# Kernel tuning notes

Measured on AMD Instinct MI355X. Metric: run time of the kernel, lower is better.

Reference implementation:

```python
import jax, jax.numpy as jnp
import numpy as np
import math

B, D_MODEL, EMB, ORDER, SEQ = 4, 64, 33, 64, 256
TARGET, FAST_PCT, SLOW_PCT = 0.01, 0.3, 1.5


def _pos_emb(L, emb_dim):
    # PositionalEmbedding: t in [0,1], complex exponential bands
    t = jnp.linspace(0.0, 1.0, L)[None, :, None]                     # [1,L,1]
    bands = (emb_dim - 1) // 2
    t_r = jnp.linspace(0.0, L - 1.0, L)[None, :, None]
    w = 2.0 * math.pi * t_r / L
    f = jnp.linspace(1e-4, bands - 1.0, bands)[None, None]
    zc = jnp.exp(-1j * f * w)
    z = jnp.concatenate([t, zc.real, zc.imag], axis=-1)              # [1,L,emb_dim]
    return z.astype(jnp.float32), t.astype(jnp.float32)


def setup_inputs() -> dict:
    key = jax.random.key(0)
    ks = jax.random.split(key, 24)
    z, _ = _pos_emb(SEQ, EMB)

    def lin(k, fan_in, fan_out):
        return jax.random.normal(k, (fan_in, fan_out), jnp.float32) / np.sqrt(fan_in)

    inp = {
        'x': jax.random.normal(ks[0], (B, D_MODEL, SEQ, SEQ), jnp.float32),
        'z': z,
        'Xw1': lin(ks[1], EMB, ORDER), 'Xb1': jax.random.normal(ks[2], (ORDER,), jnp.float32) * 0.02,
        'Xw2': lin(ks[3], ORDER, ORDER), 'Xb2': jax.random.normal(ks[4], (ORDER,), jnp.float32) * 0.02,
        'Xw3': lin(ks[5], ORDER, ORDER), 'Xb3': jax.random.normal(ks[6], (ORDER,), jnp.float32) * 0.02,
        'Xwo': lin(ks[7], ORDER, D_MODEL),
        'Xfreq': jnp.ones((1, ORDER), jnp.float32),  # Sin freq, w=1, shared across layers
        'Yw1': lin(ks[8], EMB, ORDER), 'Yb1': jax.random.normal(ks[9], (ORDER,), jnp.float32) * 0.02,
        'Yw2': lin(ks[10], ORDER, ORDER), 'Yb2': jax.random.normal(ks[11], (ORDER,), jnp.float32) * 0.02,
        'Yw3': lin(ks[12], ORDER, ORDER), 'Yb3': jax.random.normal(ks[13], (ORDER,), jnp.float32) * 0.02,
        'Ywo': lin(ks[14], ORDER, D_MODEL),
        'Yfreq': jnp.ones((1, ORDER), jnp.float32),
        'bias': jax.random.normal(ks[15], (D_MODEL,), jnp.float32),
        'L': SEQ,
    }
    return inp


def _implicit_filter(z, w1, b1, w2, b2, w3, b3, wo, freq, t, deltas):
    # MLP with shared Sin activation, then exponential modulation (shift=0)
    h = jnp.sin(freq * (z @ w1 + b1))
    h = jnp.sin(freq * (h @ w2 + b2))
    h = jnp.sin(freq * (h @ w3 + b3))
    h = h @ wo                                   # [1,L,d_model]
    decay = jnp.exp(-t * jnp.abs(deltas))        # [1,L,d_model]
    return h * decay


def reference(x, z, Xw1, Xb1, Xw2, Xb2, Xw3, Xb3, Xwo, Xfreq,
              Yw1, Yb1, Yw2, Yb2, Yw3, Yb3, Ywo, Yfreq, bias, L):
    d_model = x.shape[1]
    t = jnp.linspace(0.0, 1.0, L)[None, :, None].astype(jnp.float32)
    max_dec = math.log(TARGET) / FAST_PCT
    min_dec = math.log(TARGET) / SLOW_PCT
    deltas = jnp.linspace(min_dec, max_dec, d_model)[None, None].astype(jnp.float32)

    hx = _implicit_filter(z, Xw1, Xb1, Xw2, Xb2, Xw3, Xb3, Xwo, Xfreq, t, deltas)
    hy = _implicit_filter(z, Yw1, Yb1, Yw2, Yb2, Yw3, Yb3, Ywo, Yfreq, t, deltas)
    # separable outer-product 2D kernel: [1,L,L,d_model] -> [d_model,L,L]
    k = jnp.einsum('ijk,imk->ijmk', hx, hy)[0]
    k = jnp.transpose(k, (2, 0, 1))

    fft_size = 2 * L
    k_f = jnp.fft.rfft2(k, s=(fft_size, fft_size)) / fft_size       # [D, 2L, L+1]
    u_f = jnp.fft.rfft2(x.astype(jnp.float32), s=(fft_size, fft_size))  # [B, D, 2L, L+1]
    y = jnp.fft.irfft2(u_f * k_f, s=(fft_size, fft_size))[..., :L, :L]
    out = y + x * bias[:, None, None]
    return out.astype(x.dtype)
```

## Files before the change

kernel.cpp:

```cpp
#include <hip/hip_runtime.h>

#define SL 256
#define RSTRIDE 312

typedef _Float16 f16;
typedef _Float16 f16x8 __attribute__((ext_vector_type(8)));
typedef _Float16 f16x4 __attribute__((ext_vector_type(4)));
typedef float f32x4 __attribute__((ext_vector_type(4)));

__global__ __launch_bounds__(64) void k_filters(
    const float* __restrict__ z,
    const float* __restrict__ Xw1, const float* __restrict__ Xb1,
    const float* __restrict__ Xw2, const float* __restrict__ Xb2,
    const float* __restrict__ Xw3, const float* __restrict__ Xb3,
    const float* __restrict__ Xwo, const float* __restrict__ Xfreq,
    const float* __restrict__ Yw1, const float* __restrict__ Yb1,
    const float* __restrict__ Yw2, const float* __restrict__ Yb2,
    const float* __restrict__ Yw3, const float* __restrict__ Yb3,
    const float* __restrict__ Ywo, const float* __restrict__ Yfreq,
    f16* __restrict__ hxT, f16* __restrict__ hyT)
{
    const int l = blockIdx.x;
    const int sel = blockIdx.y;
    const int t = threadIdx.x;
    const float* w1 = sel ? Yw1 : Xw1;  const float* b1 = sel ? Yb1 : Xb1;
    const float* w2 = sel ? Yw2 : Xw2;  const float* b2 = sel ? Yb2 : Xb2;
    const float* w3 = sel ? Yw3 : Xw3;  const float* b3 = sel ? Yb3 : Xb3;
    const float* wo = sel ? Ywo : Xwo;  const float* freq = sel ? Yfreq : Xfreq;
    f16* hT = sel ? hyT : hxT;

    __shared__ float zb[33];
    __shared__ float ha[64];
    __shared__ float hb[64];

    if (t < 33) zb[t] = z[l * 33 + t];
    __syncthreads();

    const float fr = freq[t];
    float s = b1[t];
    for (int k = 0; k < 33; ++k) s += zb[k] * w1[k * 64 + t];
    ha[t] = sinf(fr * s);
    __syncthreads();

    s = b2[t];
    for (int k = 0; k < 64; ++k) s += ha[k] * w2[k * 64 + t];
    hb[t] = sinf(fr * s);
    __syncthreads();

    s = b3[t];
    for (int k = 0; k < 64; ++k) s += hb[k] * w3[k * 64 + t];
    ha[t] = sinf(fr * s);
    __syncthreads();

    s = 0.f;
    for (int k = 0; k < 64; ++k) s += ha[k] * wo[k * 64 + t];

    const float MIN_DEC = -3.0701134573253937f;
    const float MAX_DEC = -15.350567286626968f;
    float ad = fabsf(MIN_DEC + (MAX_DEC - MIN_DEC) * ((float)t / 63.0f));
    float tl = (float)l / 255.0f;
    hT[t * 256 + l] = (f16)(s * expf(-tl * ad));
}

__device__ __forceinline__ f16x8 cvt8(float4 a, float4 b)
{
    f16x8 h;
    h[0] = (f16)a.x; h[1] = (f16)a.y; h[2] = (f16)a.z; h[3] = (f16)a.w;
    h[4] = (f16)b.x; h[5] = (f16)b.y; h[6] = (f16)b.z; h[7] = (f16)b.w;
    return h;
}

__device__ __forceinline__ void build_R(f16* R, const f16* __restrict__ hc,
                                        int tid)
{
    for (int idx = tid; idx < 8 * RSTRIDE; idx += 512) {
        int c = idx / RSTRIDE;
        int k = idx - c * RSTRIDE;
        int u = k + c;
        R[idx] = (u <= 255) ? hc[255 - u] : (f16)0.f;
    }
}

template<int J0>
__device__ __forceinline__ void phase1(
    const float* __restrict__ xr0, const float* __restrict__ xr1,
    const f16* __restrict__ R, f32x4 (&acc)[16], int ln, int quad)
{
    constexpr int QS = (J0 == 0) ? 4 : 8;
    float4 a0 = *(const float4*)xr0;
    float4 a1 = *(const float4*)(xr0 + 4);
    float4 b0 = *(const float4*)xr1;
    float4 b1 = *(const float4*)(xr1 + 4);

#pragma unroll
    for (int s = 0; s < QS; ++s) {
        const int q0 = s * 32;
        f16x8 af0 = cvt8(a0, a1);
        f16x8 af1 = cvt8(b0, b1);
        if (s + 1 < QS) {
            a0 = *(const float4*)(xr0 + q0 + 32);
            a1 = *(const float4*)(xr0 + q0 + 36);
            b0 = *(const float4*)(xr1 + q0 + 32);
            b1 = *(const float4*)(xr1 + q0 + 36);
        }
#pragma unroll
        for (int c8 = 0; c8 < 8; ++c8) {
            if (32 * s <= J0 + c8 * 16 + 15) {
                int j = J0 + c8 * 16 + ln;
                int s0 = 255 - j + q0 + quad * 8;
                int c = s0 & 7;
                f16x8 bf = *(const f16x8*)&R[c * RSTRIDE + (s0 - c)];
                acc[c8] = __builtin_amdgcn_mfma_f32_16x16x32_f16(
                    af0, bf, acc[c8], 0, 0, 0);
                acc[8 + c8] = __builtin_amdgcn_mfma_f32_16x16x32_f16(
                    af1, bf, acc[8 + c8], 0, 0, 0);
            }
        }
    }
}

__global__ __launch_bounds__(512, 4) void k_fused(
    const float* __restrict__ x, const f16* __restrict__ hxT,
    const f16* __restrict__ hyT, const float* __restrict__ bias,
    float* __restrict__ out)
{
    const int bd = blockIdx.x & 255;
    const int j0 = (blockIdx.x >> 8) << 7;
    const int d  = bd & 63;
    const int tid  = threadIdx.x;
    const int lane = tid & 63;
    const int wave = tid >> 6;
    const int ln   = lane & 15;
    const int quad = lane >> 4;

    __shared__ __align__(16) f16 tmp[128 * 256];
    __shared__ __align__(16) f16 Ry[8 * RSTRIDE];
    __shared__ __align__(16) f16 Rx[8 * RSTRIDE];

    const float* xbd = x + (size_t)bd * (SL * SL);

    build_R(Ry, hyT + d * 256, tid);
    build_R(Rx, hxT + d * 256, tid);

    f32x4 acc[16];
#pragma unroll
    for (int a = 0; a < 16; ++a) acc[a] = (f32x4){0.f, 0.f, 0.f, 0.f};

    __syncthreads();

    {
        const float* xr0 = xbd + (wave * 32 + ln) * SL + quad * 8;
        const float* xr1 = xr0 + 16 * SL;
        if (j0 == 0) phase1<0>(xr0, xr1, Ry, acc, ln, quad);
        else         phase1<128>(xr0, xr1, Ry, acc, ln, quad);

#pragma unroll
        for (int r = 0; r < 2; ++r)
#pragma unroll
            for (int c8 = 0; c8 < 8; ++c8) {
                int jl = c8 * 16 + ln;
                int pb = wave * 32 + r * 16 + quad * 4;
                f32x4 a = acc[r * 8 + c8];
                f16x4 v;
                v[0] = (f16)a[0]; v[1] = (f16)a[1];
                v[2] = (f16)a[2]; v[3] = (f16)a[3];
                *(f16x4*)&tmp[jl * 256 + (pb ^ ((jl & 7) << 3))] = v;
            }
    }

#pragma unroll
    for (int a = 0; a < 16; ++a) acc[a] = (f32x4){0.f, 0.f, 0.f, 0.f};

    __syncthreads();

    const int igrp = wave & 3;
    const int jgrp = wave >> 2;
    const int nst = (igrp + 1) * 2;
    const float bv = bias[d];
    const float sc = 1.0f / 512.0f;
    float* obd = out + (size_t)bd * (SL * SL);

    for (int s = 0; s < nst; ++s) {
        const int p0 = s * 32;
        f16x8 af[4];
#pragma unroll
        for (int rt = 0; rt < 4; ++rt) {
            int jl = jgrp * 64 + rt * 16 + ln;
            int off = (p0 + quad * 8) ^ ((jl & 7) << 3);
            af[rt] = *(const f16x8*)&tmp[jl * 256 + off];
        }
#pragma unroll
        for (int ct = 0; ct < 4; ++ct) {
            if (p0 <= igrp * 64 + ct * 16 + 15) {
                int i = igrp * 64 + ct * 16 + ln;
                int s0 = 255 - i + p0 + quad * 8;
                int c = s0 & 7;
                f16x8 bf = *(const f16x8*)&Rx[c * RSTRIDE + (s0 - c)];
#pragma unroll
                for (int rt = 0; rt < 4; ++rt)
                    acc[rt * 4 + ct] = __builtin_amdgcn_mfma_f32_16x16x32_f16(
                        af[rt], bf, acc[rt * 4 + ct], 0, 0, 0);
            }
        }
#pragma unroll
        for (int ct = 0; ct < 4; ++ct) {
            int sd = (igrp * 64 + ct * 16 + 15) >> 5;
            if (s == sd) {
                int i = igrp * 64 + ct * 16 + ln;
#pragma unroll
                for (int rt = 0; rt < 4; ++rt) {
                    int j = j0 + jgrp * 64 + rt * 16 + quad * 4;
                    f32x4 a = acc[rt * 4 + ct];
                    float4 xv = *(const float4*)(xbd + i * SL + j);
                    float4 o;
                    o.x = a[0] * sc + xv.x * bv;
                    o.y = a[1] * sc + xv.y * bv;
                    o.z = a[2] * sc + xv.z * bv;
                    o.w = a[3] * sc + xv.w * bv;
                    *(float4*)(obd + i * SL + j) = o;
                }
            }
        }
    }
}

extern "C" void kernel_launch(void* const* d_in, const int* in_sizes, int n_in,
                              void* d_out, int out_size, void* d_ws, size_t ws_size,
                              hipStream_t stream)
{
    (void)in_sizes; (void)n_in; (void)out_size; (void)ws_size;
    const float* x     = (const float*)d_in[0];
    const float* z     = (const float*)d_in[1];
    const float* Xw1   = (const float*)d_in[2];
    const float* Xb1   = (const float*)d_in[3];
    const float* Xw2   = (const float*)d_in[4];
    const float* Xb2   = (const float*)d_in[5];
    const float* Xw3   = (const float*)d_in[6];
    const float* Xb3   = (const float*)d_in[7];
    const float* Xwo   = (const float*)d_in[8];
    const float* Xfreq = (const float*)d_in[9];
    const float* Yw1   = (const float*)d_in[10];
    const float* Yb1   = (const float*)d_in[11];
    const float* Yw2   = (const float*)d_in[12];
    const float* Yb2   = (const float*)d_in[13];
    const float* Yw3   = (const float*)d_in[14];
    const float* Yb3   = (const float*)d_in[15];
    const float* Ywo   = (const float*)d_in[16];
    const float* Yfreq = (const float*)d_in[17];
    const float* bias  = (const float*)d_in[18];

    f16* hxT = (f16*)d_ws;
    f16* hyT = hxT + 64 * 256;

    k_filters<<<dim3(256, 2), 64, 0, stream>>>(
        z, Xw1, Xb1, Xw2, Xb2, Xw3, Xb3, Xwo, Xfreq,
        Yw1, Yb1, Yw2, Yb2, Yw3, Yb3, Ywo, Yfreq, hxT, hyT);
    k_fused<<<512, 512, 0, stream>>>(x, hxT, hyT, bias, (float*)d_out);
}
```

Measured before the change: 178.2 us.

## Split fused 2D convolution into two kernels with a global f16 intermediate

When the workspace is large enough, the single fused kernel is replaced by two kernels. The first runs the row-direction Toeplitz MFMA pass and writes an f16 intermediate M to global memory. The second reads M, runs the column pass and applies bias and scale. Dropping the large LDS staging buffer lets more blocks fit per CU, at the cost of an extra 32 MB write and read through global memory or cache. The fallback fused kernel now reuses one R buffer for both filters to cut LDS, and moves its output stores after the main loop.

```diff
diff --git a/kernel.cpp b/kernel.cpp
--- a/kernel.cpp
+++ b/kernel.cpp
@@ -119,10 +119,9 @@
     }
 }
 
-__global__ __launch_bounds__(512, 4) void k_fused(
-    const float* __restrict__ x, const f16* __restrict__ hxT,
-    const f16* __restrict__ hyT, const float* __restrict__ bias,
-    float* __restrict__ out)
+__global__ __launch_bounds__(512, 4) void k_conv1(
+    const float* __restrict__ x, const f16* __restrict__ hyT,
+    f16* __restrict__ M)
 {
     const int bd = blockIdx.x & 255;
     const int j0 = (blockIdx.x >> 8) << 7;
@@ -133,14 +132,125 @@
     const int ln   = lane & 15;
     const int quad = lane >> 4;
 
+    __shared__ __align__(16) f16 Ry[8 * RSTRIDE];
+    build_R(Ry, hyT + d * 256, tid);
+
+    f32x4 acc[16];
+#pragma unroll
+    for (int a = 0; a < 16; ++a) acc[a] = (f32x4){0.f, 0.f, 0.f, 0.f};
+
+    __syncthreads();
+
+    const float* xr0 = x + (size_t)bd * (SL * SL) + (wave * 32 + ln) * SL + quad * 8;
+    const float* xr1 = xr0 + 16 * SL;
+    if (j0 == 0) phase1<0>(xr0, xr1, Ry, acc, ln, quad);
+    else         phase1<128>(xr0, xr1, Ry, acc, ln, quad);
+
+    f16* Mb = M + (size_t)bd * (SL * SL);
+#pragma unroll
+    for (int r = 0; r < 2; ++r)
+#pragma unroll
+        for (int c8 = 0; c8 < 8; ++c8) {
+            int jl = j0 + c8 * 16 + ln;
+            int pb = wave * 32 + r * 16 + quad * 4;
+            f32x4 a = acc[r * 8 + c8];
+            f16x4 v;
+            v[0] = (f16)a[0]; v[1] = (f16)a[1];
+            v[2] = (f16)a[2]; v[3] = (f16)a[3];
+            *(f16x4*)&Mb[jl * 256 + pb] = v;
+        }
+}
+
+__global__ __launch_bounds__(512, 4) void k_conv2(
+    const float* __restrict__ x, const f16* __restrict__ M,
+    const f16* __restrict__ hxT, const float* __restrict__ bias,
+    float* __restrict__ out)
+{
+    const int bd = blockIdx.x & 255;
+    const int jh = blockIdx.x >> 8;
+    const int d  = bd & 63;
+    const int tid  = threadIdx.x;
+    const int lane = tid & 63;
+    const int wave = tid >> 6;
+    const int ln   = lane & 15;
+    const int quad = lane >> 4;
+
+    __shared__ __align__(16) f16 Rx[8 * RSTRIDE];
+    build_R(Rx, hxT + d * 256, tid);
+
+    f32x4 acc[16];
+#pragma unroll
+    for (int a = 0; a < 16; ++a) acc[a] = (f32x4){0.f, 0.f, 0.f, 0.f};
+
+    __syncthreads();
+
+    const int igrp = wave & 3;
+    const int jgrp = wave >> 2;
+    const f16* Mb = M + (size_t)bd * (SL * SL) + (size_t)(jh * 128 + jgrp * 64) * 256;
+    const int nst = (igrp + 1) * 2;
+
+    for (int s = 0; s < nst; ++s) {
+        const int p0 = s * 32;
+        f16x8 af[4];
+#pragma unroll
+        for (int rt = 0; rt < 4; ++rt)
+            af[rt] = *(const f16x8*)&Mb[(rt * 16 + ln) * 256 + p0 + quad * 8];
+#pragma unroll
+        for (int ct = 0; ct < 4; ++ct) {
+            if (p0 <= igrp * 64 + ct * 16 + 15) {
+                int i = igrp * 64 + ct * 16 + ln;
+                int s0 = 255 - i + p0 + quad * 8;
+                int c = s0 & 7;
+                f16x8 bf = *(const f16x8*)&Rx[c * RSTRIDE + (s0 - c)];
+#pragma unroll
+                for (int rt = 0; rt < 4; ++rt)
+                    acc[rt * 4 + ct] = __builtin_amdgcn_mfma_f32_16x16x32_f16(
+                        af[rt], bf, acc[rt * 4 + ct], 0, 0, 0);
+            }
+        }
+    }
+
+    const float bv = bias[d];
+    const float sc = 1.0f / 512.0f;
+    const float* xbd = x + (size_t)bd * (SL * SL);
+    float* obd = out + (size_t)bd * (SL * SL);
+#pragma unroll
+    for (int rt = 0; rt < 4; ++rt)
+#pragma unroll
+        for (int ct = 0; ct < 4; ++ct) {
+            int i = igrp * 64 + ct * 16 + ln;
+            int j = jh * 128 + jgrp * 64 + rt * 16 + quad * 4;
+            f32x4 a = acc[rt * 4 + ct];
+            float4 xv = *(const float4*)(xbd + i * SL + j);
+            float4 o;
+            o.x = a[0] * sc + xv.x * bv;
+            o.y = a[1] * sc + xv.y * bv;
+            o.z = a[2] * sc + xv.z * bv;
+            o.w = a[3] * sc + xv.w * bv;
+            *(float4*)(obd + i * SL + j) = o;
+        }
+}
+
+__global__ __launch_bounds__(512, 4) void k_fused(
+    const float* __restrict__ x, const f16* __restrict__ hxT,
+    const f16* __restrict__ hyT, const float* __restrict__ bias,
+    float* __restrict__ out)
+{
+    const int bd = blockIdx.x & 255;
+    const int j0 = (blockIdx.x >> 8) << 7;
+    const int d  = bd & 63;
+    const int tid  = threadIdx.x;
+    const int lane = tid & 63;
+    const int wave = tid >> 6;
+    const int ln   = lane & 15;
+    const int quad = lane >> 4;
+
     __shared__ __align__(16) f16 tmp[128 * 256];
-    __shared__ __align__(16) f16 Ry[8 * RSTRIDE];
-    __shared__ __align__(16) f16 Rx[8 * RSTRIDE];
+    __shared__ __align__(16) f16 R[8 * RSTRIDE];
 
     const float* xbd = x + (size_t)bd * (SL * SL);
 
-    build_R(Ry, hyT + d * 256, tid);
-    build_R(Rx, hxT + d * 256, tid);
+    build_R(R, hyT + d * 256, tid);
 
     f32x4 acc[16];
 #pragma unroll
@@ -151,8 +261,8 @@
     {
         const float* xr0 = xbd + (wave * 32 + ln) * SL + quad * 8;
         const float* xr1 = xr0 + 16 * SL;
-        if (j0 == 0) phase1<0>(xr0, xr1, Ry, acc, ln, quad);
-        else         phase1<128>(xr0, xr1, Ry, acc, ln, quad);
+        if (j0 == 0) phase1<0>(xr0, xr1, R, acc, ln, quad);
+        else         phase1<128>(xr0, xr1, R, acc, ln, quad);
 
 #pragma unroll
         for (int r = 0; r < 2; ++r)
@@ -168,18 +278,15 @@
             }
     }
 
+    __syncthreads();
+    build_R(R, hxT + d * 256, tid);
 #pragma unroll
     for (int a = 0; a < 16; ++a) acc[a] = (f32x4){0.f, 0.f, 0.f, 0.f};
-
     __syncthreads();
 
     const int igrp = wave & 3;
     const int jgrp = wave >> 2;
     const int nst = (igrp + 1) * 2;
-    const float bv = bias[d];
-    const float sc = 1.0f / 512.0f;
-    float* obd = out + (size_t)bd * (SL * SL);
-
     for (int s = 0; s < nst; ++s) {
         const int p0 = s * 32;
         f16x8 af[4];
@@ -195,40 +302,40 @@
                 int i = igrp * 64 + ct * 16 + ln;
                 int s0 = 255 - i + p0 + quad * 8;
                 int c = s0 & 7;
-                f16x8 bf = *(const f16x8*)&Rx[c * RSTRIDE + (s0 - c)];
+                f16x8 bf = *(const f16x8*)&R[c * RSTRIDE + (s0 - c)];
 #pragma unroll
                 for (int rt = 0; rt < 4; ++rt)
                     acc[rt * 4 + ct] = __builtin_amdgcn_mfma_f32_16x16x32_f16(
                         af[rt], bf, acc[rt * 4 + ct], 0, 0, 0);
             }
         }
+    }
+
+    const float bv = bias[d];
+    const float sc = 1.0f / 512.0f;
+    float* obd = out + (size_t)bd * (SL * SL);
+#pragma unroll
+    for (int rt = 0; rt < 4; ++rt)
 #pragma unroll
         for (int ct = 0; ct < 4; ++ct) {
-            int sd = (igrp * 64 + ct * 16 + 15) >> 5;
-            if (s == sd) {
-                int i = igrp * 64 + ct * 16 + ln;
-#pragma unroll
-                for (int rt = 0; rt < 4; ++rt) {
-                    int j = j0 + jgrp * 64 + rt * 16 + quad * 4;
-                    f32x4 a = acc[rt * 4 + ct];
-                    float4 xv = *(const float4*)(xbd + i * SL + j);
-                    float4 o;
-                    o.x = a[0] * sc + xv.x * bv;
-                    o.y = a[1] * sc + xv.y * bv;
-                    o.z = a[2] * sc + xv.z * bv;
-                    o.w = a[3] * sc + xv.w * bv;
-                    *(float4*)(obd + i * SL + j) = o;
-                }
-            }
-        }
-    }
+            int i = igrp * 64 + ct * 16 + ln;
+            int j = j0 + jgrp * 64 + rt * 16 + quad * 4;
+            f32x4 a = acc[rt * 4 + ct];
+            float4 xv = *(const float4*)(xbd + i * SL + j);
+            float4 o;
+            o.x = a[0] * sc + xv.x * bv;
+            o.y = a[1] * sc + xv.y * bv;
+            o.z = a[2] * sc + xv.z * bv;
+            o.w = a[3] * sc + xv.w * bv;
+            *(float4*)(obd + i * SL + j) = o;
+        }
 }
 
 extern "C" void kernel_launch(void* const* d_in, const int* in_sizes, int n_in,
                               void* d_out, int out_size, void* d_ws, size_t ws_size,
                               hipStream_t stream)
 {
-    (void)in_sizes; (void)n_in; (void)out_size; (void)ws_size;
+    (void)in_sizes; (void)n_in; (void)out_size;
     const float* x     = (const float*)d_in[0];
     const float* z     = (const float*)d_in[1];
     const float* Xw1   = (const float*)d_in[2];
@@ -251,9 +358,18 @@
 
     f16* hxT = (f16*)d_ws;
     f16* hyT = hxT + 64 * 256;
+    const size_t filt_bytes = 2u * 64 * 256 * sizeof(f16);
+    const size_t M_bytes    = (size_t)256 * 256 * 256 * sizeof(f16);
 
     k_filters<<<dim3(256, 2), 64, 0, stream>>>(
         z, Xw1, Xb1, Xw2, Xb2, Xw3, Xb3, Xwo, Xfreq,
         Yw1, Yb1, Yw2, Yb2, Yw3, Yb3, Ywo, Yfreq, hxT, hyT);
-    k_fused<<<512, 512, 0, stream>>>(x, hxT, hyT, bias, (float*)d_out);
-}
+
+    if (ws_size >= filt_bytes + M_bytes) {
+        f16* M = (f16*)((char*)d_ws + filt_bytes);
+        k_conv1<<<512, 512, 0, stream>>>(x, hyT, M);
+        k_conv2<<<512, 512, 0, stream>>>(x, M, hxT, bias, (float*)d_out);
+    } else {
+        k_fused<<<512, 512, 0, stream>>>(x, hxT, hyT, bias, (float*)d_out);
+    }
+}
```

Measured after the change: 191.0 us. 1.07x slower.
